# Kernel tuning notes

Hardware: AMD Instinct MI355X
Metric: run time of the kernel (lower is better)

The kernel has to match this reference:

```python
import jax, jax.numpy as jnp
import numpy as np

B, T0, H0, W0 = 8, 32, 16, 16
DV, DA, NH = 1024, 512, 16
L2 = 2048
EPS = 1e-6


def setup_inputs() -> dict:
    key = jax.random.key(0)
    ks = jax.random.split(key, 16)
    s = 0.02
    inp = {
        "video_x": jax.random.normal(ks[0], (B, T0 * H0 * W0, DV), jnp.float32),
        "audio_x": jax.random.normal(ks[1], (B, L2, DA), jnp.float32),
        "probe": jax.random.normal(ks[2], (1, 1, DV), jnp.float32) * s,
        "wq": jax.random.normal(ks[3], (DV, DV), jnp.float32) * s,
        "wk": jax.random.normal(ks[4], (DV, DV), jnp.float32) * s,
        "wv": jax.random.normal(ks[5], (DV, DV), jnp.float32) * s,
        "bq": jnp.zeros((DV,), jnp.float32),
        "bk": jnp.zeros((DV,), jnp.float32),
        "bv": jnp.zeros((DV,), jnp.float32),
        "wo": jax.random.normal(ks[6], (DV, DV), jnp.float32) * s,
        "bo": jnp.zeros((DV,), jnp.float32),
        "ln_g": jnp.ones((DV,), jnp.float32),
        "ln_b": jnp.zeros((DV,), jnp.float32),
        "proj_w": jax.random.normal(ks[7], (DA, DV), jnp.float32) * s,
        "proj_b": jnp.zeros((DA,), jnp.float32),
        "logit_scale": jnp.array([3.0], jnp.float32),
        "logit_bias": jnp.array([-3.9], jnp.float32),
        "T": T0, "H": H0, "W": W0,
    }
    return inp


def reference(video_x, audio_x, probe, wq, wk, wv, bq, bk, bv, wo, bo,
              ln_g, ln_b, proj_w, proj_b, logit_scale, logit_bias, T, H, W):
    Bv, L1, D = video_x.shape
    S = H * W
    dh = D // NH
    x = video_x.reshape(Bv, T, S, D)
    # single probe query, shared across B*T: project once
    q = (probe[0, 0] @ wq.T + bq).reshape(NH, dh)                      # [h,dh]
    k = (jnp.einsum('btsd,ed->btse', x, wk) + bk).reshape(Bv, T, S, NH, dh)
    v = (jnp.einsum('btsd,ed->btse', x, wv) + bv).reshape(Bv, T, S, NH, dh)
    scores = jnp.einsum('hd,btshd->bthcaptured'[:0] or 0, k) if False else jnp.einsum('hd,btshd->btsh', q, k) / jnp.sqrt(jnp.float32(dh))
    attn = jax.nn.softmax(scores, axis=2)                              # over S
    ctx = jnp.einsum('btsh,btshd->bthd', attn, v).reshape(Bv, T, D)
    pooled = ctx @ wo.T + bo                                           # [B,T,D]
    # LayerNorm
    mu = pooled.mean(-1, keepdims=True)
    var = ((pooled - mu) ** 2).mean(-1, keepdims=True)
    pooled = (pooled - mu) / jnp.sqrt(var + EPS) * ln_g + ln_b
    # project to audio dim, L2-normalize both sides
    vt = pooled @ proj_w.T + proj_b                                    # [B,T,Da]
    vt = vt / jnp.linalg.norm(vt, axis=-1, keepdims=True)
    a = audio_x / jnp.linalg.norm(audio_x, axis=-1, keepdims=True)
    sim = jnp.einsum('btd,bld->btl', vt, a)
    return sim * jnp.exp(logit_scale[0]) + logit_bias[0]
```

## Files before the change

### kernel.cpp

```cpp
#include <hip/hip_runtime.h>


#define FB_QWT    0u
#define FB_QB     16384u
#define FB_QF     16400u
#define FB_CTXX   18432u
#define FB_CTXP   4212736u
#define FB_POOLP  4737024u
#define FB_LNO    5261312u
#define FB_VTP    5523456u
#define FB_FLOATS 5785600u

typedef __attribute__((ext_vector_type(8))) short short8v;
typedef __attribute__((ext_vector_type(4))) float float4v;

__device__ __forceinline__ void bar_lds() {
    asm volatile("s_waitcnt lgkmcnt(0)\n\ts_barrier" ::: "memory");
}

__global__ __launch_bounds__(256) void k_qflat(const float* __restrict__ probe,
                                               const float* __restrict__ wq,
                                               const float* __restrict__ bq,
                                               float* __restrict__ qf) {
    int e = blockIdx.x, tid = threadIdx.x;
    const float* wr = wq + (size_t)e * 1024;
    float s = 0.f;
    for (int k = tid; k < 1024; k += 256) s += probe[k] * wr[k];
    s += __shfl_xor(s, 1);  s += __shfl_xor(s, 2);  s += __shfl_xor(s, 4);
    s += __shfl_xor(s, 8);  s += __shfl_xor(s, 16); s += __shfl_xor(s, 32);
    __shared__ float sm[4];
    if ((tid & 63) == 0) sm[tid >> 6] = s;
    __syncthreads();
    if (tid == 0) qf[e] = sm[0] + sm[1] + sm[2] + sm[3] + bq[e];
}

__global__ __launch_bounds__(64) void k_qwt(const float* __restrict__ qf,
                                            const float* __restrict__ wk,
                                            const float* __restrict__ bk,
                                            float* __restrict__ qwt_hd,
                                            float* __restrict__ qbs) {
    int kc = blockIdx.x, h = blockIdx.y, tid = threadIdx.x;
    int d = kc * 64 + tid;
    float s = 0.f;
    for (int e0 = 0; e0 < 64; ++e0) {
        int e = h * 64 + e0;
        s += qf[e] * wk[(size_t)e * 1024 + d];
    }
    qwt_hd[h * 1024 + d] = s * 0.125f;
    if (kc == 0) {
        float p = qf[h * 64 + tid] * bk[h * 64 + tid];
        p += __shfl_xor(p, 1);  p += __shfl_xor(p, 2);  p += __shfl_xor(p, 4);
        p += __shfl_xor(p, 8);  p += __shfl_xor(p, 16); p += __shfl_xor(p, 32);
        if (tid == 0) qbs[h] = p * 0.125f;
    }
}

__device__ __forceinline__ unsigned bf_rne(float f) {
    unsigned u = __float_as_uint(f);
    return (u + 0x7FFFu + ((u >> 16) & 1u)) >> 16;
}
__device__ __forceinline__ uint2 pack_bf4(float4 v) {
    uint2 r;
    r.x = bf_rne(v.x) | (bf_rne(v.y) << 16);
    r.y = bf_rne(v.z) | (bf_rne(v.w) << 16);
    return r;
}

__global__ __launch_bounds__(512, 2) void k1_attn(const float* __restrict__ x,
                                                  const float* __restrict__ qwt_hd,
                                                  const float* __restrict__ qbs,
                                                  float* __restrict__ ctxx) {
    __shared__ __align__(16) unsigned short xbf[16][1056];
    __shared__ __align__(16) unsigned short qwbf[16][1056];
    __shared__ __align__(16) float part[8][16][16];
    __shared__ __align__(16) float p_lds[16][16];
    __shared__ float qb_lds[16];
    __shared__ float linv_lds[16];

    const int tid  = threadIdx.x;
    const int lane = tid & 63;
    const int w    = tid >> 6;
    const int hq   = tid >> 7;
    const int cc   = tid & 127;
    const int bt   = blockIdx.x;
    const float* xb = x + (size_t)bt * 262144;

#pragma unroll
    for (int i = 0; i < 8; ++i) {
        int f4i = tid + i * 512;
        int hr = f4i >> 8, col4 = f4i & 255;
        float4 v = *(const float4*)(qwt_hd + hr * 1024 + col4 * 4);
        *(uint2*)&qwbf[hr][col4 * 4] = pack_bf4(v);
    }
    if (tid < 16) qb_lds[tid] = qbs[tid];

    float lacc = 0.f;
    float4 acc[8];
#pragma unroll
    for (int i = 0; i < 8; ++i) acc[i] = make_float4(0.f, 0.f, 0.f, 0.f);

    float4 st[8];
#pragma unroll
    for (int i = 0; i < 8; ++i)
        st[i] = *(const float4*)(xb + (size_t)(tid + i * 512) * 4);

    for (int c = 0; c < 16; ++c) {
        bar_lds();
#pragma unroll
        for (int i = 0; i < 8; ++i) {
            int f4i = tid + i * 512;
            int r = f4i >> 8, col4 = f4i & 255;
            *(uint2*)&xbf[r][col4 * 4] = pack_bf4(st[i]);
        }
        if (c < 15) {
            const float* nb = xb + (size_t)(c + 1) * 16384;
#pragma unroll
            for (int i = 0; i < 8; ++i)
                st[i] = *(const float4*)(nb + (size_t)(tid + i * 512) * 4);
        }
        bar_lds();
        {
            const int row = lane & 15;
            const int g   = lane >> 4;
            float4v cfr = {0.f, 0.f, 0.f, 0.f};
#pragma unroll
            for (int ks = 0; ks < 4; ++ks) {
                const int koff = (w * 4 + ks) * 32 + g * 8;
                short8v afr = *(const short8v*)&xbf[row][koff];
                short8v bfr = *(const short8v*)&qwbf[row][koff];
                cfr = __builtin_amdgcn_mfma_f32_16x16x32_bf16(afr, bfr, cfr, 0, 0, 0);
            }
#pragma unroll
            for (int r2 = 0; r2 < 4; ++r2)
                part[w][(lane >> 4) * 4 + r2][lane & 15] = cfr[r2];
        }
        bar_lds();
        if (tid < 256) {
            int s = tid >> 4, h = tid & 15;
            float sc = 0.f;
#pragma unroll
            for (int pw = 0; pw < 8; ++pw) sc += part[pw][s][h];
            p_lds[s][h] = __expf(sc + qb_lds[h]);
        }
        bar_lds();
        if (tid < 16) {
            float ll = 0.f;
#pragma unroll
            for (int s = 0; s < 16; ++s) ll += p_lds[s][tid];
            lacc += ll;
        }
#pragma unroll
        for (int r = 0; r < 16; ++r) {
            uint4 xv = *(const uint4*)&xbf[r][cc * 8];
            float x0 = __uint_as_float(xv.x << 16);
            float x1 = __uint_as_float(xv.x & 0xFFFF0000u);
            float x2 = __uint_as_float(xv.y << 16);
            float x3 = __uint_as_float(xv.y & 0xFFFF0000u);
            float x4 = __uint_as_float(xv.z << 16);
            float x5 = __uint_as_float(xv.z & 0xFFFF0000u);
            float x6 = __uint_as_float(xv.w << 16);
            float x7 = __uint_as_float(xv.w & 0xFFFF0000u);
            float4 p4 = *(const float4*)&p_lds[r][hq * 4];
            acc[0].x += p4.x * x0; acc[0].y += p4.x * x1; acc[0].z += p4.x * x2; acc[0].w += p4.x * x3;
            acc[1].x += p4.y * x0; acc[1].y += p4.y * x1; acc[1].z += p4.y * x2; acc[1].w += p4.y * x3;
            acc[2].x += p4.z * x0; acc[2].y += p4.z * x1; acc[2].z += p4.z * x2; acc[2].w += p4.z * x3;
            acc[3].x += p4.w * x0; acc[3].y += p4.w * x1; acc[3].z += p4.w * x2; acc[3].w += p4.w * x3;
            acc[4].x += p4.x * x4; acc[4].y += p4.x * x5; acc[4].z += p4.x * x6; acc[4].w += p4.x * x7;
            acc[5].x += p4.y * x4; acc[5].y += p4.y * x5; acc[5].z += p4.y * x6; acc[5].w += p4.y * x7;
            acc[6].x += p4.z * x4; acc[6].y += p4.z * x5; acc[6].z += p4.z * x6; acc[6].w += p4.z * x7;
            acc[7].x += p4.w * x4; acc[7].y += p4.w * x5; acc[7].z += p4.w * x6; acc[7].w += p4.w * x7;
        }
    }

    bar_lds();
    if (tid < 16) linv_lds[tid] = 1.0f / lacc;
    bar_lds();
    float* ob = ctxx + (size_t)bt * 16384;
#pragma unroll
    for (int i = 0; i < 4; ++i) {
        float li = linv_lds[hq * 4 + i];
        float4 o0 = acc[i];
        float4 o1 = acc[4 + i];
        o0.x *= li; o0.y *= li; o0.z *= li; o0.w *= li;
        o1.x *= li; o1.y *= li; o1.z *= li; o1.w *= li;
        float* dst = ob + (hq * 4 + i) * 1024 + cc * 8;
        *(float4*)dst = o0;
        *(float4*)(dst + 4) = o1;
    }
}

template<int FOLD>
__global__ __launch_bounds__(256, 2) void k_gemm2(const float* __restrict__ A0,
                                                  const float* __restrict__ A1,
                                                  const float* __restrict__ biask,
                                                  const float* __restrict__ Bw,
                                                  float* __restrict__ outp,
                                                  unsigned a_rstride, unsigned a_cstride,
                                                  unsigned ostride) {
    __shared__ __align__(16) float a_s[16][68];
    __shared__ __align__(16) float b_s[64][68];
    const int tid = threadIdx.x;
    const int rc = blockIdx.x;
    const int cb = blockIdx.y;
    const int ks = blockIdx.z;
    const int koff = ks * 512;
    const int rr = tid >> 4;
    const int ee = tid & 15;

    const size_t abase = (size_t)(rc * 16 + rr) * a_rstride + (size_t)cb * a_cstride + koff;

    float ac0 = 0.f, ac1 = 0.f, ac2 = 0.f, ac3 = 0.f;

    for (int kc = 0; kc < 8; ++kc) {
        __syncthreads();
        {
            float4 av = *(const float4*)(A0 + abase + kc * 64 + ee * 4);
            if (FOLD == 1) {
                float4 a1v = *(const float4*)(A1 + abase + kc * 64 + ee * 4);
                float4 bk4 = *(const float4*)(biask + koff + kc * 64 + ee * 4);
                av.x += a1v.x + bk4.x; av.y += a1v.y + bk4.y;
                av.z += a1v.z + bk4.z; av.w += a1v.w + bk4.w;
            }
            *(float4*)&a_s[rr][ee * 4] = av;
        }
#pragma unroll
        for (int i = 0; i < 4; ++i) {
            int f4i = tid + i * 256;
            int e = f4i >> 4, k4 = f4i & 15;
            float4 bv4 = *(const float4*)(Bw + (size_t)(cb * 64 + e) * 1024 + koff + kc * 64 + k4 * 4);
            int cs = (k4 + (e >> 2)) & 15;
            *(float4*)&b_s[e][cs * 4] = bv4;
        }
        __syncthreads();
#pragma unroll
        for (int k4 = 0; k4 < 16; ++k4) {
            float4 av = *(const float4*)&a_s[rr][k4 * 4];
            int cs = (k4 + ee) & 15;
            float4 b0 = *(const float4*)&b_s[ee * 4 + 0][cs * 4];
            float4 b1 = *(const float4*)&b_s[ee * 4 + 1][cs * 4];
            float4 b2 = *(const float4*)&b_s[ee * 4 + 2][cs * 4];
            float4 b3 = *(const float4*)&b_s[ee * 4 + 3][cs * 4];
            ac0 += av.x * b0.x + av.y * b0.y + av.z * b0.z + av.w * b0.w;
            ac1 += av.x * b1.x + av.y * b1.y + av.z * b1.z + av.w * b1.w;
            ac2 += av.x * b2.x + av.y * b2.y + av.z * b2.z + av.w * b2.w;
            ac3 += av.x * b3.x + av.y * b3.y + av.z * b3.z + av.w * b3.w;
        }
    }
    float4 o = make_float4(ac0, ac1, ac2, ac3);
    *(float4*)(outp + (size_t)ks * 256 * ostride + (size_t)(rc * 16 + rr) * ostride + cb * 64 + ee * 4) = o;
}

__global__ __launch_bounds__(256) void k_ln(const float* __restrict__ poolp,
                                            const float* __restrict__ bo,
                                            const float* __restrict__ g,
                                            const float* __restrict__ bb,
                                            float* __restrict__ out) {
    __shared__ float sm[8];
    int row = blockIdx.x, tid = threadIdx.x;
    float4 v0 = *(const float4*)(poolp + (size_t)row * 1024 + tid * 4);
    float4 v1 = *(const float4*)(poolp + 262144u + (size_t)row * 1024 + tid * 4);
    float4 bv = *(const float4*)(bo + tid * 4);
    float4 v;
    v.x = v0.x + v1.x + bv.x; v.y = v0.y + v1.y + bv.y;
    v.z = v0.z + v1.z + bv.z; v.w = v0.w + v1.w + bv.w;
    float s = v.x + v.y + v.z + v.w;
    float q = v.x * v.x + v.y * v.y + v.z * v.z + v.w * v.w;
    s += __shfl_xor(s, 1);  q += __shfl_xor(q, 1);
    s += __shfl_xor(s, 2);  q += __shfl_xor(q, 2);
    s += __shfl_xor(s, 4);  q += __shfl_xor(q, 4);
    s += __shfl_xor(s, 8);  q += __shfl_xor(q, 8);
    s += __shfl_xor(s, 16); q += __shfl_xor(q, 16);
    s += __shfl_xor(s, 32); q += __shfl_xor(q, 32);
    if ((tid & 63) == 0) { sm[tid >> 6] = s; sm[4 + (tid >> 6)] = q; }
    __syncthreads();
    float S = sm[0] + sm[1] + sm[2] + sm[3];
    float Q = sm[4] + sm[5] + sm[6] + sm[7];
    float mu = S * (1.f / 1024.f);
    float var = Q * (1.f / 1024.f) - mu * mu;
    float rs = rsqrtf(var + 1e-6f);
    float4 gg = *(const float4*)(g + tid * 4);
    float4 be = *(const float4*)(bb + tid * 4);
    float4 o;
    o.x = (v.x - mu) * rs * gg.x + be.x;
    o.y = (v.y - mu) * rs * gg.y + be.y;
    o.z = (v.z - mu) * rs * gg.z + be.z;
    o.w = (v.w - mu) * rs * gg.w + be.w;
    *(float4*)(out + (size_t)row * 1024 + tid * 4) = o;
}

__global__ __launch_bounds__(256, 2) void k_sim(const float* __restrict__ vtp,
                                                const float* __restrict__ pb,
                                                const float* __restrict__ audio,
                                                const float* __restrict__ ls,
                                                const float* __restrict__ lb,
                                                float* __restrict__ out) {
    __shared__ float a_s[64][65];
    __shared__ float v_s[32][65];
    __shared__ float rinv_a[64];
    __shared__ float rinv_v[32];
    const int tid = threadIdx.x;
    const int lc = blockIdx.x;
    const int b  = blockIdx.y;
    const int al = tid >> 2, ak = (tid & 3) * 16;
    const int vl = tid >> 3, vk = (tid & 7) * 8;
    const int rg = tid >> 4, lg = tid & 15;
    float ssa = 0.f, ssv = 0.f;
    float c00=0,c01=0,c02=0,c03=0,c10=0,c11=0,c12=0,c13=0;

    for (int kc = 0; kc < 8; ++kc) {
        __syncthreads();
        {
            const float* ap = audio + (size_t)b * 1048576 + (size_t)(lc * 64 + al) * 512 + kc * 64 + ak;
#pragma unroll
            for (int i = 0; i < 4; ++i) {
                float4 wv4 = *(const float4*)(ap + i * 4);
                ssa += wv4.x * wv4.x + wv4.y * wv4.y + wv4.z * wv4.z + wv4.w * wv4.w;
                a_s[al][ak + i * 4 + 0] = wv4.x; a_s[al][ak + i * 4 + 1] = wv4.y;
                a_s[al][ak + i * 4 + 2] = wv4.z; a_s[al][ak + i * 4 + 3] = wv4.w;
            }
            const size_t voff = (size_t)(b * 32 + vl) * 512 + kc * 64 + vk;
#pragma unroll
            for (int i = 0; i < 2; ++i) {
                float4 p0 = *(const float4*)(vtp + voff + i * 4);
                float4 p1 = *(const float4*)(vtp + 131072u + voff + i * 4);
                float4 pbv = *(const float4*)(pb + kc * 64 + vk + i * 4);
                float4 wv4;
                wv4.x = p0.x + p1.x + pbv.x; wv4.y = p0.y + p1.y + pbv.y;
                wv4.z = p0.z + p1.z + pbv.z; wv4.w = p0.w + p1.w + pbv.w;
                ssv += wv4.x * wv4.x + wv4.y * wv4.y + wv4.z * wv4.z + wv4.w * wv4.w;
                v_s[vl][vk + i * 4 + 0] = wv4.x; v_s[vl][vk + i * 4 + 1] = wv4.y;
                v_s[vl][vk + i * 4 + 2] = wv4.z; v_s[vl][vk + i * 4 + 3] = wv4.w;
            }
        }
        __syncthreads();
#pragma unroll 2
        for (int k = 0; k < 64; ++k) {
            float v0 = v_s[rg * 2 + 0][k];
            float v1 = v_s[rg * 2 + 1][k];
            float x0 = a_s[lg * 4 + 0][k];
            float x1 = a_s[lg * 4 + 1][k];
            float x2 = a_s[lg * 4 + 2][k];
            float x3 = a_s[lg * 4 + 3][k];
            c00 += v0 * x0; c01 += v0 * x1; c02 += v0 * x2; c03 += v0 * x3;
            c10 += v1 * x0; c11 += v1 * x1; c12 += v1 * x2; c13 += v1 * x3;
        }
    }
    ssa += __shfl_xor(ssa, 1); ssa += __shfl_xor(ssa, 2);
    if ((tid & 3) == 0) rinv_a[al] = rsqrtf(ssa);
    ssv += __shfl_xor(ssv, 1); ssv += __shfl_xor(ssv, 2); ssv += __shfl_xor(ssv, 4);
    if ((tid & 7) == 0) rinv_v[vl] = rsqrtf(ssv);
    __syncthreads();
    const float sc = __expf(ls[0]);
    const float bias = lb[0];
    float ra0 = rinv_a[lg * 4 + 0], ra1 = rinv_a[lg * 4 + 1];
    float ra2 = rinv_a[lg * 4 + 2], ra3 = rinv_a[lg * 4 + 3];
    float accs[2][4] = {{c00,c01,c02,c03},{c10,c11,c12,c13}};
#pragma unroll
    for (int cr = 0; cr < 2; ++cr) {
        int t = rg * 2 + cr;
        float rv = rinv_v[t] * sc;
        float4 o;
        o.x = accs[cr][0] * rv * ra0 + bias;
        o.y = accs[cr][1] * rv * ra1 + bias;
        o.z = accs[cr][2] * rv * ra2 + bias;
        o.w = accs[cr][3] * rv * ra3 + bias;
        *(float4*)(out + (size_t)b * 65536 + (size_t)t * 2048 + lc * 64 + lg * 4) = o;
    }
}

extern "C" void kernel_launch(void* const* d_in, const int* in_sizes, int n_in,
                              void* d_out, int out_size, void* d_ws, size_t ws_size,
                              hipStream_t stream) {
    (void)in_sizes; (void)n_in; (void)out_size;
    const float* video = (const float*)d_in[0];
    const float* audio = (const float*)d_in[1];
    const float* probe = (const float*)d_in[2];
    const float* wq    = (const float*)d_in[3];
    const float* wk    = (const float*)d_in[4];
    const float* wv    = (const float*)d_in[5];
    const float* bq    = (const float*)d_in[6];
    const float* bk    = (const float*)d_in[7];
    const float* bv    = (const float*)d_in[8];
    const float* wo    = (const float*)d_in[9];
    const float* bo    = (const float*)d_in[10];
    const float* lng   = (const float*)d_in[11];
    const float* lnb   = (const float*)d_in[12];
    const float* pw    = (const float*)d_in[13];
    const float* pb    = (const float*)d_in[14];
    const float* ls    = (const float*)d_in[15];
    const float* lb    = (const float*)d_in[16];
    float* ws  = (float*)d_ws;
    float* out = (float*)d_out;
    if (ws_size < FB_FLOATS * sizeof(float)) return;

    float* qwt  = ws + FB_QWT;
    float* qbs  = ws + FB_QB;
    float* qf   = ws + FB_QF;
    float* ctxx = ws + FB_CTXX;
    float* ctxp = ws + FB_CTXP;
    float* poolp= ws + FB_POOLP;
    float* lno  = ws + FB_LNO;
    float* vtp  = ws + FB_VTP;

    k_qflat<<<dim3(1024), dim3(256), 0, stream>>>(probe, wq, bq, qf);
    k_qwt<<<dim3(16, 16), dim3(64), 0, stream>>>(qf, wk, bk, qwt, qbs);
    k1_attn<<<dim3(256), dim3(512), 0, stream>>>(video, qwt, qbs, ctxx);
    k_gemm2<0><<<dim3(16, 16, 2), dim3(256), 0, stream>>>(ctxx, nullptr, nullptr, wv, ctxp,
                                                          16384u, 1024u, 1024u);
    k_gemm2<1><<<dim3(16, 16, 2), dim3(256), 0, stream>>>(ctxp, ctxp + 262144u, bv, wo, poolp,
                                                          1024u, 0u, 1024u);
    k_ln<<<dim3(256), dim3(256), 0, stream>>>(poolp, bo, lng, lnb, lno);
    k_gemm2<0><<<dim3(16, 8, 2), dim3(256), 0, stream>>>(lno, nullptr, nullptr, pw, vtp,
                                                         1024u, 0u, 512u);
    k_sim<<<dim3(32, 8), dim3(256), 0, stream>>>(vtp, pb, audio, ls, lb, out);
}
```

Baseline: 173.4 us.

## Swizzle bf16 LDS tiles in attention kernel and store context as bf16

Applies an XOR swizzle to the column index of the bf16 x and q-weight LDS tiles in the attention kernel, so MFMA fragment loads and the row-wise context reads spread across more LDS banks. The per-(b,t) context output is now written as packed bf16 rather than fp32, which halves that intermediate's global traffic. The first value-projection GEMM gains a template flag to read and unpack bf16 A operands. This costs a little precision in the context tensor.

```diff
diff --git a/kernel.cpp b/kernel.cpp
--- a/kernel.cpp
+++ b/kernel.cpp
@@ -17,6 +17,8 @@
 __device__ __forceinline__ void bar_lds() {
     asm volatile("s_waitcnt lgkmcnt(0)\n\ts_barrier" ::: "memory");
 }
+
+#define SW(R, C) ((C) ^ (((R) & 7) << 3))
 
 __global__ __launch_bounds__(256) void k_qflat(const float* __restrict__ probe,
                                                const float* __restrict__ wq,
@@ -90,7 +92,7 @@
         int f4i = tid + i * 512;
         int hr = f4i >> 8, col4 = f4i & 255;
         float4 v = *(const float4*)(qwt_hd + hr * 1024 + col4 * 4);
-        *(uint2*)&qwbf[hr][col4 * 4] = pack_bf4(v);
+        *(uint2*)&qwbf[hr][SW(hr, col4 * 4)] = pack_bf4(v);
     }
     if (tid < 16) qb_lds[tid] = qbs[tid];
 
@@ -110,7 +112,7 @@
         for (int i = 0; i < 8; ++i) {
             int f4i = tid + i * 512;
             int r = f4i >> 8, col4 = f4i & 255;
-            *(uint2*)&xbf[r][col4 * 4] = pack_bf4(st[i]);
+            *(uint2*)&xbf[r][SW(r, col4 * 4)] = pack_bf4(st[i]);
         }
         if (c < 15) {
             const float* nb = xb + (size_t)(c + 1) * 16384;
@@ -126,8 +128,8 @@
 #pragma unroll
             for (int ks = 0; ks < 4; ++ks) {
                 const int koff = (w * 4 + ks) * 32 + g * 8;
-                short8v afr = *(const short8v*)&xbf[row][koff];
-                short8v bfr = *(const short8v*)&qwbf[row][koff];
+                short8v afr = *(const short8v*)&xbf[row][SW(row, koff)];
+                short8v bfr = *(const short8v*)&qwbf[row][SW(row, koff)];
                 cfr = __builtin_amdgcn_mfma_f32_16x16x32_bf16(afr, bfr, cfr, 0, 0, 0);
             }
 #pragma unroll
@@ -151,7 +153,7 @@
         }
 #pragma unroll
         for (int r = 0; r < 16; ++r) {
-            uint4 xv = *(const uint4*)&xbf[r][cc * 8];
+            uint4 xv = *(const uint4*)&xbf[r][SW(r, cc * 8)];
             float x0 = __uint_as_float(xv.x << 16);
             float x1 = __uint_as_float(xv.x & 0xFFFF0000u);
             float x2 = __uint_as_float(xv.y << 16);
@@ -175,7 +177,7 @@
     bar_lds();
     if (tid < 16) linv_lds[tid] = 1.0f / lacc;
     bar_lds();
-    float* ob = ctxx + (size_t)bt * 16384;
+    unsigned short* ob = (unsigned short*)ctxx + (size_t)bt * 16384;
 #pragma unroll
     for (int i = 0; i < 4; ++i) {
         float li = linv_lds[hq * 4 + i];
@@ -183,13 +185,14 @@
         float4 o1 = acc[4 + i];
         o0.x *= li; o0.y *= li; o0.z *= li; o0.w *= li;
         o1.x *= li; o1.y *= li; o1.z *= li; o1.w *= li;
-        float* dst = ob + (hq * 4 + i) * 1024 + cc * 8;
-        *(float4*)dst = o0;
-        *(float4*)(dst + 4) = o1;
-    }
-}
-
-template<int FOLD>
+        uint2 p0 = pack_bf4(o0);
+        uint2 p1 = pack_bf4(o1);
+        uint4 pk = make_uint4(p0.x, p0.y, p1.x, p1.y);
+        *(uint4*)(ob + (hq * 4 + i) * 1024 + cc * 8) = pk;
+    }
+}
+
+template<int FOLD, int ABF16>
 __global__ __launch_bounds__(256, 2) void k_gemm2(const float* __restrict__ A0,
                                                   const float* __restrict__ A1,
                                                   const float* __restrict__ biask,
@@ -214,7 +217,17 @@
     for (int kc = 0; kc < 8; ++kc) {
         __syncthreads();
         {
-            float4 av = *(const float4*)(A0 + abase + kc * 64 + ee * 4);
+            float4 av;
+            if (ABF16) {
+                const unsigned short* A0h = (const unsigned short*)A0;
+                uint2 u = *(const uint2*)(A0h + abase + kc * 64 + ee * 4);
+                av.x = __uint_as_float(u.x << 16);
+                av.y = __uint_as_float(u.x & 0xFFFF0000u);
+                av.z = __uint_as_float(u.y << 16);
+                av.w = __uint_as_float(u.y & 0xFFFF0000u);
+            } else {
+                av = *(const float4*)(A0 + abase + kc * 64 + ee * 4);
+            }
             if (FOLD == 1) {
                 float4 a1v = *(const float4*)(A1 + abase + kc * 64 + ee * 4);
                 float4 bk4 = *(const float4*)(biask + koff + kc * 64 + ee * 4);
@@ -405,12 +418,12 @@
     k_qflat<<<dim3(1024), dim3(256), 0, stream>>>(probe, wq, bq, qf);
     k_qwt<<<dim3(16, 16), dim3(64), 0, stream>>>(qf, wk, bk, qwt, qbs);
     k1_attn<<<dim3(256), dim3(512), 0, stream>>>(video, qwt, qbs, ctxx);
-    k_gemm2<0><<<dim3(16, 16, 2), dim3(256), 0, stream>>>(ctxx, nullptr, nullptr, wv, ctxp,
-                                                          16384u, 1024u, 1024u);
-    k_gemm2<1><<<dim3(16, 16, 2), dim3(256), 0, stream>>>(ctxp, ctxp + 262144u, bv, wo, poolp,
-                                                          1024u, 0u, 1024u);
+    k_gemm2<0, 1><<<dim3(16, 16, 2), dim3(256), 0, stream>>>(ctxx, nullptr, nullptr, wv, ctxp,
+                                                             16384u, 1024u, 1024u);
+    k_gemm2<1, 0><<<dim3(16, 16, 2), dim3(256), 0, stream>>>(ctxp, ctxp + 262144u, bv, wo, poolp,
+                                                             1024u, 0u, 1024u);
     k_ln<<<dim3(256), dim3(256), 0, stream>>>(poolp, bo, lng, lnb, lno);
-    k_gemm2<0><<<dim3(16, 8, 2), dim3(256), 0, stream>>>(lno, nullptr, nullptr, pw, vtp,
-                                                         1024u, 0u, 512u);
+    k_gemm2<0, 0><<<dim3(16, 8, 2), dim3(256), 0, stream>>>(lno, nullptr, nullptr, pw, vtp,
+                                                            1024u, 0u, 512u);
     k_sim<<<dim3(32, 8), dim3(256), 0, stream>>>(vtp, pb, audio, ls, lb, out);
 }
```

Result: no change. 172.9 us (-0.3%).
